# Kernel optimization log

Hardware: AMD Instinct MI355X
Metric: run time of the kernel (lower is better)

## Reference

```python
import jax, jax.numpy as jnp
import numpy as np

EPS = 1e-5
B, F, C, H, L, S = 8192, 128, 256, 512, 4, 10


def _gelu(x):
    return jax.nn.gelu(x, approximate=False)  # torch nn.GELU default = exact erf


def _ln(x, g, b):
    m = jnp.mean(x, axis=-1, keepdims=True)
    v = jnp.var(x, axis=-1, keepdims=True)  # biased, matches torch LayerNorm
    return (x - m) / jnp.sqrt(v + EPS) * g + b


def setup_inputs() -> dict:
    key = jax.random.key(0)
    ks = iter(jax.random.split(key, 40))

    def w(shape, fan_in):
        return jax.random.normal(next(ks), shape, jnp.float32) / np.float32(np.sqrt(fan_in))

    def z0(*s):
        return jnp.zeros(s, jnp.float32)

    return dict(
        x=jax.random.normal(next(ks), (B, F), jnp.float32),
        context=jax.random.normal(next(ks), (B, C), jnp.float32),
        u=jax.random.normal(next(ks), (S, B, F), jnp.float32),
        Wi=w((F, H), F), bi=z0(H),
        Wt1=w((1, H), 1), bt1=z0(H), Wt2=w((H, H), H), bt2=z0(H),
        Wc1=w((C, 2 * H), C), bc1=z0(2 * H), Wc2=w((2 * H, H), 2 * H), bc2=z0(H),
        Wv=w((L, H, H), H), bv=z0(L, H), Woa=w((L, H, H), H), boa=z0(L, H),
        g1=jnp.ones((L, H), jnp.float32), be1=z0(L, H),
        Wm1=w((L, H, 4 * H), H), bm1=z0(L, 4 * H),
        Wm2=w((L, 4 * H, H), 4 * H), bm2=z0(L, H),
        g2=jnp.ones((L, H), jnp.float32), be2=z0(L, H),
        Wcv=w((L, H, H), H), bcv=z0(L, H), Wco=w((L, H, H), H), bco=z0(L, H),
        scale=0.5 * jnp.ones((L,), jnp.float32),
        Wp1=w((H, H), H), bp1=z0(H), Wp2=w((H, F), H), bp2=z0(F),
    )


def _forward(x, context, u, Wi, bi, Wt1, bt1, Wt2, bt2, Wc1, bc1, Wc2, bc2,
             Wv, bv, Woa, boa, g1, be1, Wm1, bm1, Wm2, bm2, g2, be2,
             Wcv, bcv, Wco, bco, scale, Wp1, bp1, Wp2, bp2):
    n_steps = u.shape[0]
    dt = 1.0 / n_steps
    nb = x.shape[0]
    nl = Wv.shape[0]

    # context projection, computed once as in torch
    ctx = _gelu(context @ Wc1 + bc1) @ Wc2 + bc2  # [B,H]
    # seq_len==1 cross-attention: softmax over a single key == 1, so the output
    # is out_proj(v_proj(ctx)) and does not depend on x -> precompute per layer.
    vctx = jnp.einsum('bh,lhk->lbk', ctx, Wcv) + bcv[:, None, :]    # [L,B,H]
    xatt = jnp.einsum('lbh,lhk->lbk', vctx, Wco) + bco[:, None, :]  # [L,B,H]

    def vel(z, t):
        tt = jnp.clip(t, 0.0, 1.0)[:, None]                          # [B,1]
        h = z @ Wi + bi + (_gelu(tt @ Wt1 + bt1) @ Wt2 + bt2)        # [B,H]
        for l in range(nl):
            # seq_len==1 self-attention collapses to out_proj(v_proj(h))
            attn = (h @ Wv[l] + bv[l]) @ Woa[l] + boa[l]
            h = _ln(h + attn, g1[l], be1[l])
            mlp = _gelu(h @ Wm1[l] + bm1[l]) @ Wm2[l] + bm2[l]
            h = _ln(h + mlp, g2[l], be2[l])
            h = h + scale[l] * xatt[l]
        return _gelu(h @ Wp1 + bp1) @ Wp2 + bp2                      # [B,F]

    def step(carry, inp):
        z, ld = carry
        t_val, u_k = inp
        t = jnp.full((nb,), t_val, jnp.float32)
        zs = jax.lax.stop_gradient(z)  # matches z.detach()/leaf z_req in torch
        v, Ju = jax.jvp(lambda zz: vel(zz, t), (zs,), (u_k,))
        ld = ld + jnp.sum(u_k * Ju, axis=-1) * dt  # Hutchinson u^T J u
        return (zs + v * dt, ld), None

    ts = jnp.arange(n_steps, dtype=jnp.float32) * dt
    (z, log_det), _ = jax.lax.scan(step, (x, jnp.zeros((nb,), jnp.float32)), (ts, u))
    return z, log_det


def reference(x, context, u, Wi, bi, Wt1, bt1, Wt2, bt2, Wc1, bc1, Wc2, bc2,
              Wv, bv, Woa, boa, g1, be1, Wm1, bm1, Wm2, bm2, g2, be2,
              Wcv, bcv, Wco, bco, scale, Wp1, bp1, Wp2, bp2):
    return _forward(x, context, u, Wi, bi, Wt1, bt1, Wt2, bt2, Wc1, bc1, Wc2, bc2,
                    Wv, bv, Woa, boa, g1, be1, Wm1, bm1, Wm2, bm2, g2, be2,
                    Wcv, bcv, Wco, bco, scale, Wp1, bp1, Wp2, bp2)
```

## Files before the change

### kernel.cpp

```cpp
#include <hip/hip_runtime.h>
#include <math.h>

using floatx16 = __attribute__((ext_vector_type(16))) float;
using bf16x8   = __attribute__((ext_vector_type(8))) __bf16;
using ushort8  = __attribute__((ext_vector_type(8))) unsigned short;

__device__ __forceinline__ float b2f(unsigned short u) {
  unsigned v = ((unsigned)u) << 16; float f; __builtin_memcpy(&f, &v, 4); return f;
}
__device__ __forceinline__ unsigned short f2b(float f) {
  unsigned u; __builtin_memcpy(&u, &f, 4);
  u += 0x7fffu + ((u >> 16) & 1u);
  return (unsigned short)(u >> 16);
}
__device__ __forceinline__ float gelu_f(float x) {
  return 0.5f * x * (1.0f + erff(x * 0.7071067811865475f));
}
__device__ __forceinline__ float wred(float v) {
  #pragma unroll
  for (int off = 32; off > 0; off >>= 1) v += __shfl_xor(v, off, 64);
  return v;
}
__device__ __forceinline__ floatx16 zero16() {
  floatx16 z;
  #pragma unroll
  for (int e = 0; e < 16; e++) z[e] = 0.f;
  return z;
}

#define SWZS(r, c) (((r) << 5) + ((((c) ^ ((r) & 3))) << 3))

template<int MODE>
__global__ __launch_bounds__(256) void gemm_bt_k(
    const unsigned short* __restrict__ A, const unsigned short* __restrict__ Bt,
    void* __restrict__ C, const float* __restrict__ bias,
    const float* __restrict__ bias2, int M, int N, int K)
{
  __shared__ unsigned short As[2 * 128 * 32];
  __shared__ unsigned short Bs[2 * 128 * 32];
  const int tid  = threadIdx.x;
  const int lane = tid & 63;
  const int wave = tid >> 6;

  int bx = blockIdx.x, by = blockIdx.y;
  if ((gridDim.y & 7) == 0) {
    int lin = by * gridDim.x + bx;
    int xcd = lin & 7;
    int w   = lin >> 3;
    by = xcd * (gridDim.y >> 3) + w / gridDim.x;
    bx = w % gridDim.x;
  }
  const int row0 = by * 128;
  const int col0 = bx * 128;

  const int r0 = lane >> 2;
  const int cj = lane & 3;
  const unsigned short* Ag = A  + (size_t)(row0 + wave * 32 + r0) * K + cj * 8;
  const unsigned short* Bg = Bt + (size_t)(col0 + wave * 32 + r0) * K + cj * 8;
  const int aw0 = SWZS(wave * 32 + r0, cj);

  const int wr = wave >> 1, wc = wave & 1;
  const int m32 = lane & 31;
  const int hi  = lane >> 5;

  floatx16 acc[2][2];
  acc[0][0] = zero16(); acc[0][1] = zero16();
  acc[1][0] = zero16(); acc[1][1] = zero16();

  ushort8 ra0, ra1, rb0, rb1;
  ra0 = *(const ushort8*)(Ag);
  ra1 = *(const ushort8*)(Ag + (size_t)16 * K);
  rb0 = *(const ushort8*)(Bg);
  rb1 = *(const ushort8*)(Bg + (size_t)16 * K);

  int p = 0;
  for (int k0 = 0; k0 < K; k0 += 32) {
    unsigned short* Ab = &As[p * 4096];
    unsigned short* Bb = &Bs[p * 4096];
    *(ushort8*)(Ab + aw0)            = ra0;
    *(ushort8*)(Ab + aw0 + 16 * 32)  = ra1;
    *(ushort8*)(Bb + aw0)            = rb0;
    *(ushort8*)(Bb + aw0 + 16 * 32)  = rb1;
    __syncthreads();
    if (k0 + 32 < K) {
      ra0 = *(const ushort8*)(Ag + k0 + 32);
      ra1 = *(const ushort8*)(Ag + (size_t)16 * K + k0 + 32);
      rb0 = *(const ushort8*)(Bg + k0 + 32);
      rb1 = *(const ushort8*)(Bg + (size_t)16 * K + k0 + 32);
    }
    bf16x8 af[2][2], bfr[2][2];
    #pragma unroll
    for (int i = 0; i < 2; i++)
      #pragma unroll
      for (int h = 0; h < 2; h++)
        af[i][h] = *(const bf16x8*)&Ab[SWZS(wr * 64 + i * 32 + m32, 2 * h + hi)];
    #pragma unroll
    for (int j = 0; j < 2; j++)
      #pragma unroll
      for (int h = 0; h < 2; h++)
        bfr[j][h] = *(const bf16x8*)&Bb[SWZS(wc * 64 + j * 32 + m32, 2 * h + hi)];
    #pragma unroll
    for (int h = 0; h < 2; h++)
      #pragma unroll
      for (int i = 0; i < 2; i++)
        #pragma unroll
        for (int j = 0; j < 2; j++)
          acc[i][j] = __builtin_amdgcn_mfma_f32_32x32x16_bf16(af[i][h], bfr[j][h], acc[i][j], 0, 0, 0);
    p ^= 1;
  }

  #pragma unroll
  for (int j = 0; j < 2; j++) {
    int col = col0 + wc * 64 + j * 32 + m32;
    float bb = bias ? bias[col] : 0.f;
    if (MODE >= 2) { if (bias2) bb += bias2[col]; }
    #pragma unroll
    for (int i = 0; i < 2; i++) {
      int rb = row0 + wr * 64 + i * 32 + 4 * hi;
      if (MODE == 3) {
        #pragma unroll
        for (int pr = 0; pr < 8; pr++) {
          int re = rb + 2 * (pr & 1) + 8 * (pr >> 1);
          float pv = acc[i][j][2 * pr] + bb;
          float tv = acc[i][j][2 * pr + 1];
          float cdf = 0.5f * (1.0f + erff(pv * 0.7071067811865475f));
          float pdf = 0.3989422804014327f * expf(-0.5f * pv * pv);
          ((unsigned short*)C)[(size_t)re * N + col]       = f2b(pv * cdf);
          ((unsigned short*)C)[(size_t)(re + 1) * N + col] = f2b((cdf + pv * pdf) * tv);
        }
      } else {
        #pragma unroll
        for (int reg = 0; reg < 16; reg++) {
          int row = rb + (reg & 3) + 8 * (reg >> 2);
          float v = acc[i][j][reg];
          if (MODE == 0 || MODE == 1) v += bb;
          if (MODE == 2) { if ((reg & 1) == 0) v += bb; }
          if (MODE == 1) v = gelu_f(v);
          ((unsigned short*)C)[(size_t)row * N + col] = f2b(v);
        }
      }
    }
  }
}

__global__ __launch_bounds__(256, 2) void gemm_wide3_k(
    const unsigned short* __restrict__ A, const unsigned short* __restrict__ Bt,
    unsigned short* __restrict__ C, const float* __restrict__ bias,
    int M, int N, int K)
{
  __shared__ unsigned short As[2 * 128 * 32];
  __shared__ unsigned short Bs[2 * 256 * 32];
  const int tid  = threadIdx.x;
  const int lane = tid & 63;
  const int wave = tid >> 6;

  int bx = blockIdx.x, by = blockIdx.y;
  if ((gridDim.y & 7) == 0) {
    int lin = by * gridDim.x + bx;
    int xcd = lin & 7;
    int w   = lin >> 3;
    by = xcd * (gridDim.y >> 3) + w / gridDim.x;
    bx = w % gridDim.x;
  }
  const int row0 = by * 128;
  const int col0 = bx * 256;

  const int r0 = lane >> 2;
  const int cj = lane & 3;
  const unsigned short* Ag = A  + (size_t)(row0 + wave * 32 + r0) * K + cj * 8;
  const unsigned short* Bg = Bt + (size_t)(col0 + wave * 64 + r0) * K + cj * 8;
  const int awr = wave * 32 + r0;
  const int bwr = wave * 64 + r0;

  const int wr = wave >> 1, wc = wave & 1;
  const int m32 = lane & 31;
  const int hi  = lane >> 5;

  floatx16 acc[2][4];
  #pragma unroll
  for (int i = 0; i < 2; i++)
    #pragma unroll
    for (int j = 0; j < 4; j++) acc[i][j] = zero16();

  ushort8 ra0, ra1, rbv[4];
  ra0 = *(const ushort8*)(Ag);
  ra1 = *(const ushort8*)(Ag + (size_t)16 * K);
  #pragma unroll
  for (int t = 0; t < 4; t++)
    rbv[t] = *(const ushort8*)(Bg + (size_t)16 * t * K);

  int p = 0;
  for (int k0 = 0; k0 < K; k0 += 32) {
    unsigned short* Ab = &As[p * 4096];
    unsigned short* Bb = &Bs[p * 8192];
    *(ushort8*)&Ab[SWZS(awr, cj)]      = ra0;
    *(ushort8*)&Ab[SWZS(awr + 16, cj)] = ra1;
    #pragma unroll
    for (int t = 0; t < 4; t++)
      *(ushort8*)&Bb[SWZS(bwr + 16 * t, cj)] = rbv[t];
    __syncthreads();
    if (k0 + 32 < K) {
      ra0 = *(const ushort8*)(Ag + k0 + 32);
      ra1 = *(const ushort8*)(Ag + (size_t)16 * K + k0 + 32);
      #pragma unroll
      for (int t = 0; t < 4; t++)
        rbv[t] = *(const ushort8*)(Bg + (size_t)16 * t * K + k0 + 32);
    }
    bf16x8 af[2][2], bfr[4][2];
    #pragma unroll
    for (int i = 0; i < 2; i++)
      #pragma unroll
      for (int h = 0; h < 2; h++)
        af[i][h] = *(const bf16x8*)&Ab[SWZS(wr * 64 + i * 32 + m32, 2 * h + hi)];
    #pragma unroll
    for (int j = 0; j < 4; j++)
      #pragma unroll
      for (int h = 0; h < 2; h++)
        bfr[j][h] = *(const bf16x8*)&Bb[SWZS(wc * 128 + j * 32 + m32, 2 * h + hi)];
    #pragma unroll
    for (int h = 0; h < 2; h++)
      #pragma unroll
      for (int i = 0; i < 2; i++)
        #pragma unroll
        for (int j = 0; j < 4; j++)
          acc[i][j] = __builtin_amdgcn_mfma_f32_32x32x16_bf16(af[i][h], bfr[j][h], acc[i][j], 0, 0, 0);
    p ^= 1;
  }

  #pragma unroll
  for (int j = 0; j < 4; j++) {
    int col = col0 + wc * 128 + j * 32 + m32;
    float bb = bias[col];
    #pragma unroll
    for (int i = 0; i < 2; i++) {
      int rb = row0 + wr * 64 + i * 32 + 4 * hi;
      #pragma unroll
      for (int pr = 0; pr < 8; pr++) {
        int re = rb + 2 * (pr & 1) + 8 * (pr >> 1);
        float pv = acc[i][j][2 * pr] + bb;
        float tv = acc[i][j][2 * pr + 1];
        float cdf = 0.5f * (1.0f + erff(pv * 0.7071067811865475f));
        float pdf = 0.3989422804014327f * expf(-0.5f * pv * pv);
        C[(size_t)re * N + col]       = f2b(pv * cdf);
        C[(size_t)(re + 1) * N + col] = f2b((cdf + pv * pdf) * tv);
      }
    }
  }
}

__global__ __launch_bounds__(256) void gemm_vout_k(
    const unsigned short* __restrict__ A, const unsigned short* __restrict__ Bt,
    const float* __restrict__ bias, const float* __restrict__ u_cur,
    const float* __restrict__ u_next, float* __restrict__ zf,
    float* __restrict__ ldb, unsigned short* __restrict__ Abuf,
    int K, float dtv)
{
  constexpr int N = 128;
  __shared__ unsigned short As[2 * 128 * 32];
  __shared__ unsigned short Bs[2 * 128 * 32];
  __shared__ float red[64][2];
  const int tid = threadIdx.x, lane = tid & 63, wave = tid >> 6;
  const int row0 = blockIdx.x * 128;

  const int r0 = lane >> 2;
  const int cj = lane & 3;
  const unsigned short* Ag = A  + (size_t)(row0 + wave * 32 + r0) * K + cj * 8;
  const unsigned short* Bg = Bt + (size_t)(wave * 32 + r0) * K + cj * 8;
  const int aw0 = SWZS(wave * 32 + r0, cj);

  const int wr = wave >> 1, wc = wave & 1;
  const int m32 = lane & 31;
  const int hi  = lane >> 5;

  floatx16 acc[2][2];
  acc[0][0] = zero16(); acc[0][1] = zero16();
  acc[1][0] = zero16(); acc[1][1] = zero16();

  ushort8 ra0, ra1, rb0, rb1;
  ra0 = *(const ushort8*)(Ag);
  ra1 = *(const ushort8*)(Ag + (size_t)16 * K);
  rb0 = *(const ushort8*)(Bg);
  rb1 = *(const ushort8*)(Bg + (size_t)16 * K);

  int p = 0;
  for (int k0 = 0; k0 < K; k0 += 32) {
    unsigned short* Ab = &As[p * 4096];
    unsigned short* Bb = &Bs[p * 4096];
    *(ushort8*)(Ab + aw0)           = ra0;
    *(ushort8*)(Ab + aw0 + 16 * 32) = ra1;
    *(ushort8*)(Bb + aw0)           = rb0;
    *(ushort8*)(Bb + aw0 + 16 * 32) = rb1;
    __syncthreads();
    if (k0 + 32 < K) {
      ra0 = *(const ushort8*)(Ag + k0 + 32);
      ra1 = *(const ushort8*)(Ag + (size_t)16 * K + k0 + 32);
      rb0 = *(const ushort8*)(Bg + k0 + 32);
      rb1 = *(const ushort8*)(Bg + (size_t)16 * K + k0 + 32);
    }
    bf16x8 af[2][2], bfr[2][2];
    #pragma unroll
    for (int i = 0; i < 2; i++)
      #pragma unroll
      for (int h = 0; h < 2; h++)
        af[i][h] = *(const bf16x8*)&Ab[SWZS(wr * 64 + i * 32 + m32, 2 * h + hi)];
    #pragma unroll
    for (int j = 0; j < 2; j++)
      #pragma unroll
      for (int h = 0; h < 2; h++)
        bfr[j][h] = *(const bf16x8*)&Bb[SWZS(wc * 64 + j * 32 + m32, 2 * h + hi)];
    #pragma unroll
    for (int h = 0; h < 2; h++)
      #pragma unroll
      for (int i = 0; i < 2; i++)
        #pragma unroll
        for (int j = 0; j < 2; j++)
          acc[i][j] = __builtin_amdgcn_mfma_f32_32x32x16_bf16(af[i][h], bfr[j][h], acc[i][j], 0, 0, 0);
    p ^= 1;
  }

  #pragma unroll
  for (int i = 0; i < 2; i++) {
    #pragma unroll
    for (int pr = 0; pr < 8; pr++) {
      int re_loc = wr * 64 + i * 32 + 4 * hi + 2 * (pr & 1) + 8 * (pr >> 1);
      size_t growe = (size_t)(row0 + re_loc);
      size_t b = growe >> 1;
      float dacc = 0.f;
      #pragma unroll
      for (int j = 0; j < 2; j++) {
        int col = wc * 64 + j * 32 + m32;
        float v  = acc[i][j][2 * pr] + bias[col];
        float Ju = acc[i][j][2 * pr + 1];
        float z = zf[b * N + col] + v * dtv;
        zf[b * N + col] = z;
        Abuf[growe * N + col] = f2b(z);
        if (u_next) Abuf[(growe + 1) * N + col] = f2b(u_next[b * N + col]);
        dacc += u_cur[b * N + col] * Ju;
      }
      #pragma unroll
      for (int off = 1; off <= 16; off <<= 1) dacc += __shfl_xor(dacc, off, 64);
      if (m32 == 0) red[re_loc >> 1][wc] = dacc;
    }
  }
  __syncthreads();
  if (tid < 64) ldb[(row0 >> 1) + tid] += (red[tid][0] + red[tid][1]) * dtv;
}

__global__ __launch_bounds__(256) void ln_jvp_k(
    unsigned short* h, const unsigned short* __restrict__ r,
    const float* __restrict__ g, const float* __restrict__ be,
    const unsigned short* __restrict__ xatt, const float* __restrict__ sc_p,
    int Bhalf, int H)
{
  int gw = (int)((blockIdx.x * blockDim.x + threadIdx.x) >> 6);
  int lane = threadIdx.x & 63;
  if (gw >= Bhalf) return;
  int c0 = lane * 8;
  size_t op = (size_t)(2 * gw) * H + c0;
  size_t ot = op + H;
  ushort8 hp = *(const ushort8*)&h[op];
  ushort8 ht = *(const ushort8*)&h[ot];
  ushort8 rp = *(const ushort8*)&r[op];
  ushort8 rt = *(const ushort8*)&r[ot];
  float xv[8], dv[8];
  float s1 = 0.f, s2 = 0.f, sd = 0.f;
  #pragma unroll
  for (int j = 0; j < 8; j++) {
    xv[j] = b2f(hp[j]) + b2f(rp[j]);
    dv[j] = b2f(ht[j]) + b2f(rt[j]);
    s1 += xv[j]; s2 += xv[j] * xv[j]; sd += dv[j];
  }
  s1 = wred(s1); s2 = wred(s2); sd = wred(sd);
  float inv = 1.0f / (float)H;
  float m = s1 * inv;
  float var = s2 * inv - m * m;
  float rstd = rsqrtf(var + 1e-5f);
  float dm = sd * inv;
  float c = 0.f;
  #pragma unroll
  for (int j = 0; j < 8; j++) c += (xv[j] - m) * dv[j];
  c = wred(c);
  float cm = c * inv * rstd;
  float sl = sc_p ? *sc_p : 0.f;
  ushort8 oy, od;
  #pragma unroll
  for (int j = 0; j < 8; j++) {
    float xh = (xv[j] - m) * rstd;
    float gg = g[c0 + j];
    float y = xh * gg + be[c0 + j];
    if (xatt) y += sl * b2f(xatt[(size_t)gw * H + c0 + j]);
    float dy = gg * rstd * (dv[j] - dm - xh * cm);
    oy[j] = f2b(y); od[j] = f2b(dy);
  }
  *(ushort8*)&h[op] = oy;
  *(ushort8*)&h[ot] = od;
}

__global__ void transpose_cast_k(const float* __restrict__ W,
                                 unsigned short* __restrict__ Wt, int K, int N)
{
  __shared__ float tile[32][33];
  size_t off = (size_t)blockIdx.z * K * N;
  const float* Wp = W + off;
  unsigned short* Wtp = Wt + off;
  int bx = blockIdx.x, by = blockIdx.y;
  int tx = threadIdx.x, ty = threadIdx.y;
  #pragma unroll
  for (int i = ty; i < 32; i += 8)
    tile[i][tx] = Wp[(size_t)(by * 32 + i) * N + bx * 32 + tx];
  __syncthreads();
  #pragma unroll
  for (int i = ty; i < 32; i += 8)
    Wtp[(size_t)(bx * 32 + i) * K + by * 32 + tx] = f2b(tile[tx][i]);
}

__global__ __launch_bounds__(256) void zero_k(float* __restrict__ p, int n) {
  int i = (int)(blockIdx.x * blockDim.x + threadIdx.x);
  if (i < n) p[i] = 0.f;
}

__global__ __launch_bounds__(256) void combine_bias_k(
    const float* __restrict__ bvp, const float* __restrict__ Wb,
    const float* __restrict__ bo, float* __restrict__ bout, int H)
{
  int out = blockIdx.x * blockDim.x + threadIdx.x;
  int l   = blockIdx.y;
  int kc  = blockIdx.z;
  const float* A2 = Wb + (size_t)l * H * H;
  float s = (kc == 0) ? bo[(size_t)l * H + out] : 0.f;
  int kend = (kc + 1) * 64;
  for (int k = kc * 64; k < kend; k++) s += bvp[(size_t)l * H + k] * A2[(size_t)k * H + out];
  atomicAdd(&bout[(size_t)l * H + out], s);
}

__global__ __launch_bounds__(256) void cast_k(const float* __restrict__ in,
                                              unsigned short* __restrict__ out, size_t n) {
  size_t i = blockIdx.x * blockDim.x + threadIdx.x;
  if (i < n) out[i] = f2b(in[i]);
}

__global__ __launch_bounds__(512) void temb_all_k(
    const float* __restrict__ Wt1, const float* __restrict__ bt1,
    const float* __restrict__ Wt2, const float* __restrict__ bt2,
    float dtv, float* __restrict__ tvecs, int H)
{
  __shared__ float e[512];
  int j = threadIdx.x;
  float t = fminf(fmaxf((float)blockIdx.x * dtv, 0.f), 1.f);
  e[j] = gelu_f(t * Wt1[j] + bt1[j]);
  __syncthreads();
  float s = bt2[j];
  for (int k = 0; k < H; k++) s += e[k] * Wt2[(size_t)k * H + j];
  tvecs[(size_t)blockIdx.x * H + j] = s;
}

__global__ __launch_bounds__(256) void init_k(
    const float* __restrict__ x, const float* __restrict__ u0,
    float* __restrict__ zf, float* __restrict__ ld,
    unsigned short* __restrict__ Abuf, int BF, int Bsz, int F)
{
  int i = (int)(blockIdx.x * blockDim.x + threadIdx.x);
  if (i < BF) {
    int r = i / F, c = i - r * F;
    float v = x[i];
    zf[i] = v;
    Abuf[(size_t)(2 * r) * F + c]     = f2b(v);
    Abuf[(size_t)(2 * r + 1) * F + c] = f2b(u0[i]);
  }
  if (i < Bsz) ld[i] = 0.f;
}

__global__ __launch_bounds__(256) void final_k(
    const float* __restrict__ zf, const float* __restrict__ ld,
    float* __restrict__ out, int BF, int Bsz)
{
  int i = (int)(blockIdx.x * blockDim.x + threadIdx.x);
  if (i < BF) out[i] = zf[i];
  if (i < Bsz) out[BF + i] = ld[i];
}

extern "C" void kernel_launch(void* const* d_in, const int* in_sizes, int n_in,
                              void* d_out, int out_size, void* d_ws, size_t ws_size,
                              hipStream_t stream) {
  constexpr int B = 8192, F = 128, C = 256, H = 512, L = 4, S = 10;
  constexpr int B2 = 2 * B;
  constexpr int BF = B * F;
  const float dtv = 1.0f / S;

  const float* x    = (const float*)d_in[0];
  const float* ctxI = (const float*)d_in[1];
  const float* u    = (const float*)d_in[2];
  const float* Wi   = (const float*)d_in[3];
  const float* bi   = (const float*)d_in[4];
  const float* Wt1  = (const float*)d_in[5];
  const float* bt1  = (const float*)d_in[6];
  const float* Wt2  = (const float*)d_in[7];
  const float* bt2  = (const float*)d_in[8];
  const float* Wc1  = (const float*)d_in[9];
  const float* bc1  = (const float*)d_in[10];
  const float* Wc2  = (const float*)d_in[11];
  const float* bc2  = (const float*)d_in[12];
  const float* Wv   = (const float*)d_in[13];
  const float* bv   = (const float*)d_in[14];
  const float* Woa  = (const float*)d_in[15];
  const float* boa  = (const float*)d_in[16];
  const float* g1   = (const float*)d_in[17];
  const float* be1  = (const float*)d_in[18];
  const float* Wm1  = (const float*)d_in[19];
  const float* bm1  = (const float*)d_in[20];
  const float* Wm2  = (const float*)d_in[21];
  const float* bm2  = (const float*)d_in[22];
  const float* g2   = (const float*)d_in[23];
  const float* be2  = (const float*)d_in[24];
  const float* Wcv  = (const float*)d_in[25];
  const float* bcv  = (const float*)d_in[26];
  const float* Wco  = (const float*)d_in[27];
  const float* bco  = (const float*)d_in[28];
  const float* scal = (const float*)d_in[29];
  const float* Wp1  = (const float*)d_in[30];
  const float* bp1  = (const float*)d_in[31];
  const float* Wp2  = (const float*)d_in[32];
  const float* bp2  = (const float*)d_in[33];

  char* wp = (char*)d_ws;
  auto alloc = [&](size_t bytes) -> void* {
    void* r = (void*)wp;
    wp += (bytes + 255) & ~(size_t)255;
    return r;
  };
  unsigned short* wWit  = (unsigned short*)alloc((size_t)H * F * 2);
  unsigned short* wWc1t = (unsigned short*)alloc((size_t)2 * H * C * 2);
  unsigned short* wWc2t = (unsigned short*)alloc((size_t)H * 2 * H * 2);
  unsigned short* wWvoT = (unsigned short*)alloc((size_t)L * H * H * 2);
  unsigned short* wCtxT = (unsigned short*)alloc((size_t)L * H * H * 2);
  unsigned short* wWm1t = (unsigned short*)alloc((size_t)L * 4 * H * H * 2);
  unsigned short* wWm2t = (unsigned short*)alloc((size_t)L * H * 4 * H * 2);
  unsigned short* wWp1t = (unsigned short*)alloc((size_t)H * H * 2);
  unsigned short* wWp2t = (unsigned short*)alloc((size_t)F * H * 2);
  unsigned short* wOaT  = (unsigned short*)alloc((size_t)L * H * H * 2);
  unsigned short* wCoT  = (unsigned short*)alloc((size_t)L * H * H * 2);
  unsigned short* wVb   = (unsigned short*)alloc((size_t)L * H * H * 2);
  unsigned short* wCvb  = (unsigned short*)alloc((size_t)L * H * H * 2);
  float* bcomb          = (float*)alloc((size_t)2 * L * H * 4);
  float* bvo  = bcomb;
  float* cbvo = bcomb + (size_t)L * H;
  float* tvecs          = (float*)alloc((size_t)S * H * 4);
  unsigned short* ctxc  = (unsigned short*)alloc((size_t)B * C * 2);
  unsigned short* Abuf  = (unsigned short*)alloc((size_t)B2 * F * 2);
  unsigned short* hbuf  = (unsigned short*)alloc((size_t)B2 * H * 2);
  unsigned short* tmp2  = (unsigned short*)alloc((size_t)B2 * H * 2);
  unsigned short* mbuf  = (unsigned short*)alloc((size_t)B2 * 4 * H * 2);
  unsigned short* xattb = (unsigned short*)alloc((size_t)L * B * H * 2);
  float* zf             = (float*)alloc((size_t)B * F * 4);
  float* ldb            = (float*)alloc((size_t)B * 4);
  (void)ws_size; (void)in_sizes; (void)n_in; (void)out_size;

  auto T = [&](const float* W, unsigned short* Wt, int K, int N, int Lz) {
    dim3 g(N / 32, K / 32, Lz);
    transpose_cast_k<<<g, dim3(32, 8), 0, stream>>>(W, Wt, K, N);
  };
  auto G = [&](int mode, const unsigned short* A, const unsigned short* Bt, void* Cc,
               const float* bias, const float* bias2, int M, int N, int K) {
    dim3 g(N / 128, M / 128);
    switch (mode) {
      case 0: gemm_bt_k<0><<<g, 256, 0, stream>>>(A, Bt, Cc, bias, bias2, M, N, K); break;
      case 1: gemm_bt_k<1><<<g, 256, 0, stream>>>(A, Bt, Cc, bias, bias2, M, N, K); break;
      case 2: gemm_bt_k<2><<<g, 256, 0, stream>>>(A, Bt, Cc, bias, bias2, M, N, K); break;
      case 3: gemm_bt_k<3><<<g, 256, 0, stream>>>(A, Bt, Cc, bias, bias2, M, N, K); break;
    }
  };

  T(Wi,  wWit,  F, H, 1);
  T(Wc1, wWc1t, C, 2 * H, 1);
  T(Wc2, wWc2t, 2 * H, H, 1);
  T(Wm1, wWm1t, H, 4 * H, L);
  T(Wm2, wWm2t, 4 * H, H, L);
  T(Wp1, wWp1t, H, H, 1);
  T(Wp2, wWp2t, H, F, 1);
  T(Woa, wOaT, H, H, L);
  T(Wco, wCoT, H, H, L);
  cast_k<<<((size_t)L * H * H + 255) / 256, 256, 0, stream>>>(Wv,  wVb,  (size_t)L * H * H);
  cast_k<<<((size_t)L * H * H + 255) / 256, 256, 0, stream>>>(Wcv, wCvb, (size_t)L * H * H);
  for (int l = 0; l < L; l++) {
    size_t o2 = (size_t)l * H * H;
    G(0, wOaT + o2, wVb  + o2, wWvoT + o2, nullptr, nullptr, H, H, H);
    G(0, wCoT + o2, wCvb + o2, wCtxT + o2, nullptr, nullptr, H, H, H);
  }
  zero_k<<<(2 * L * H + 255) / 256, 256, 0, stream>>>(bcomb, 2 * L * H);
  combine_bias_k<<<dim3(H / 256, L, H / 64), 256, 0, stream>>>(bv,  Woa, boa, bvo,  H);
  combine_bias_k<<<dim3(H / 256, L, H / 64), 256, 0, stream>>>(bcv, Wco, bco, cbvo, H);

  cast_k<<<(B * C + 255) / 256, 256, 0, stream>>>(ctxI, ctxc, (size_t)B * C);
  G(1, ctxc, wWc1t, mbuf, bc1, nullptr, B, 2 * H, C);
  G(0, mbuf, wWc2t, tmp2, bc2, nullptr, B, H, 2 * H);
  for (int l = 0; l < L; l++)
    G(0, tmp2, wCtxT + (size_t)l * H * H, xattb + (size_t)l * B * H,
      cbvo + l * H, nullptr, B, H, H);

  temb_all_k<<<S, H, 0, stream>>>(Wt1, bt1, Wt2, bt2, dtv, tvecs, H);
  init_k<<<(BF + 255) / 256, 256, 0, stream>>>(x, u, zf, ldb, Abuf, BF, B, F);

  for (int s = 0; s < S; s++) {
    G(2, Abuf, wWit, hbuf, bi, tvecs + (size_t)s * H, B2, H, F);
    for (int l = 0; l < L; l++) {
      size_t o2 = (size_t)l * H * H;
      size_t om = (size_t)l * 4 * H * H;
      G(2, hbuf, wWvoT + o2, tmp2, bvo + l * H, nullptr, B2, H, H);
      ln_jvp_k<<<B / 4, 256, 0, stream>>>(hbuf, tmp2, g1 + l * H, be1 + l * H,
                                          nullptr, nullptr, B, H);
      gemm_wide3_k<<<dim3(4 * H / 256, B2 / 128), 256, 0, stream>>>(
          hbuf, wWm1t + om, mbuf, bm1 + (size_t)l * 4 * H, B2, 4 * H, H);
      G(2, mbuf, wWm2t + om, tmp2, bm2 + l * H, nullptr, B2, H, 4 * H);
      ln_jvp_k<<<B / 4, 256, 0, stream>>>(hbuf, tmp2, g2 + l * H, be2 + l * H,
                                          xattb + (size_t)l * B * H, scal + l, B, H);
    }
    G(3, hbuf, wWp1t, tmp2, bp1, nullptr, B2, H, H);
    const float* u_cur = u + (size_t)s * BF;
    const float* u_next = (s + 1 < S) ? u + (size_t)(s + 1) * BF : nullptr;
    gemm_vout_k<<<B2 / 128, 256, 0, stream>>>(
        tmp2, wWp2t, bp2, u_cur, u_next, zf, ldb, Abuf, H, dtv);
  }

  final_k<<<(BF + 255) / 256, 256, 0, stream>>>(zf, ldb, (float*)d_out, BF, B);
}
```

Baseline: 8.459 ms.

## Pre-tile weights into swizzled LDS image and load B via global_load_lds

```diff
diff --git a/kernel.cpp b/kernel.cpp
--- a/kernel.cpp
+++ b/kernel.cpp
@@ -27,10 +27,16 @@
   for (int e = 0; e < 16; e++) z[e] = 0.f;
   return z;
 }
+__device__ __forceinline__ void gload16(const unsigned short* g, unsigned short* l) {
+  __builtin_amdgcn_global_load_lds(
+      (__attribute__((address_space(1))) void*)(g),
+      (__attribute__((address_space(3))) void*)(l), 16, 0, 0);
+}
 
 #define SWZS(r, c) (((r) << 5) + ((((c) ^ ((r) & 3))) << 3))
 
-template<int MODE>
+
+template<int MODE, int IMG>
 __global__ __launch_bounds__(256) void gemm_bt_k(
     const unsigned short* __restrict__ A, const unsigned short* __restrict__ Bt,
     void* __restrict__ C, const float* __restrict__ bias,
@@ -55,9 +61,14 @@
 
   const int r0 = lane >> 2;
   const int cj = lane & 3;
-  const unsigned short* Ag = A  + (size_t)(row0 + wave * 32 + r0) * K + cj * 8;
-  const unsigned short* Bg = Bt + (size_t)(col0 + wave * 32 + r0) * K + cj * 8;
+  const unsigned short* Ag = A + (size_t)(row0 + wave * 32 + r0) * K + cj * 8;
   const int aw0 = SWZS(wave * 32 + r0, cj);
+
+  const int ks = K >> 5;
+  size_t bimg0 = 0;
+  const unsigned short* Bg = nullptr;
+  if (IMG) bimg0 = ((size_t)(col0 >> 7) * ks) * 4096 + (size_t)(wave * 2) * 512 + lane * 8;
+  else     Bg = Bt + (size_t)(col0 + wave * 32 + r0) * K + cj * 8;
 
   const int wr = wave >> 1, wc = wave & 1;
   const int m32 = lane & 31;
@@ -70,23 +81,38 @@
   ushort8 ra0, ra1, rb0, rb1;
   ra0 = *(const ushort8*)(Ag);
   ra1 = *(const ushort8*)(Ag + (size_t)16 * K);
-  rb0 = *(const ushort8*)(Bg);
-  rb1 = *(const ushort8*)(Bg + (size_t)16 * K);
+  if (IMG) {
+    gload16(Bt + bimg0,       &Bs[0] + (wave * 2) * 512);
+    gload16(Bt + bimg0 + 512, &Bs[0] + (wave * 2 + 1) * 512);
+  } else {
+    rb0 = *(const ushort8*)(Bg);
+    rb1 = *(const ushort8*)(Bg + (size_t)16 * K);
+  }
 
   int p = 0;
   for (int k0 = 0; k0 < K; k0 += 32) {
     unsigned short* Ab = &As[p * 4096];
     unsigned short* Bb = &Bs[p * 4096];
-    *(ushort8*)(Ab + aw0)            = ra0;
-    *(ushort8*)(Ab + aw0 + 16 * 32)  = ra1;
-    *(ushort8*)(Bb + aw0)            = rb0;
-    *(ushort8*)(Bb + aw0 + 16 * 32)  = rb1;
+    *(ushort8*)(Ab + aw0)           = ra0;
+    *(ushort8*)(Ab + aw0 + 16 * 32) = ra1;
+    if (!IMG) {
+      *(ushort8*)(Bb + aw0)           = rb0;
+      *(ushort8*)(Bb + aw0 + 16 * 32) = rb1;
+    }
     __syncthreads();
     if (k0 + 32 < K) {
+      if (IMG) {
+        size_t o = bimg0 + (size_t)((k0 >> 5) + 1) * 4096;
+        unsigned short* Bn = &Bs[(p ^ 1) * 4096];
+        gload16(Bt + o,       Bn + (wave * 2) * 512);
+        gload16(Bt + o + 512, Bn + (wave * 2 + 1) * 512);
+      }
       ra0 = *(const ushort8*)(Ag + k0 + 32);
       ra1 = *(const ushort8*)(Ag + (size_t)16 * K + k0 + 32);
-      rb0 = *(const ushort8*)(Bg + k0 + 32);
-      rb1 = *(const ushort8*)(Bg + (size_t)16 * K + k0 + 32);
+      if (!IMG) {
+        rb0 = *(const ushort8*)(Bg + k0 + 32);
+        rb1 = *(const ushort8*)(Bg + (size_t)16 * K + k0 + 32);
+      }
     }
     bf16x8 af[2][2], bfr[2][2];
     #pragma unroll
@@ -112,8 +138,9 @@
   #pragma unroll
   for (int j = 0; j < 2; j++) {
     int col = col0 + wc * 64 + j * 32 + m32;
-    float bb = bias ? bias[col] : 0.f;
-    if (MODE >= 2) { if (bias2) bb += bias2[col]; }
+    float bb = 0.f;
+    if (MODE != 5) { if (bias) bb = bias[col]; }
+    if (MODE >= 2 && MODE != 5) { if (bias2) bb += bias2[col]; }
     #pragma unroll
     for (int i = 0; i < 2; i++) {
       int rb = row0 + wr * 64 + i * 32 + 4 * hi;
@@ -128,6 +155,16 @@
           ((unsigned short*)C)[(size_t)re * N + col]       = f2b(pv * cdf);
           ((unsigned short*)C)[(size_t)(re + 1) * N + col] = f2b((cdf + pv * pdf) * tv);
         }
+      } else if (MODE == 5) {
+        int kc = N >> 5;
+        #pragma unroll
+        for (int reg = 0; reg < 16; reg++) {
+          int row = rb + (reg & 3) + 8 * (reg >> 2);
+          size_t off = ((size_t)(row >> 7) * kc + (col >> 5)) * 4096
+                     + (size_t)((row & 127) << 5)
+                     + ((((col >> 3) & 3) ^ (row & 3)) << 3) + (col & 7);
+          ((unsigned short*)C)[off] = f2b(acc[i][j][reg]);
+        }
       } else {
         #pragma unroll
         for (int reg = 0; reg < 16; reg++) {
@@ -167,10 +204,12 @@
 
   const int r0 = lane >> 2;
   const int cj = lane & 3;
-  const unsigned short* Ag = A  + (size_t)(row0 + wave * 32 + r0) * K + cj * 8;
-  const unsigned short* Bg = Bt + (size_t)(col0 + wave * 64 + r0) * K + cj * 8;
-  const int awr = wave * 32 + r0;
-  const int bwr = wave * 64 + r0;
+  const unsigned short* Ag = A + (size_t)(row0 + wave * 32 + r0) * K + cj * 8;
+  const int awr = SWZS(wave * 32 + r0, cj);
+
+  const int ks = K >> 5;
+  const size_t bq0 = ((size_t)((col0 >> 7) + 0) * ks) * 4096 + (size_t)(wave * 2) * 512 + lane * 8;
+  const size_t bq1 = ((size_t)((col0 >> 7) + 1) * ks) * 4096 + (size_t)(wave * 2) * 512 + lane * 8;
 
   const int wr = wave >> 1, wc = wave & 1;
   const int m32 = lane & 31;
@@ -182,29 +221,32 @@
     #pragma unroll
     for (int j = 0; j < 4; j++) acc[i][j] = zero16();
 
-  ushort8 ra0, ra1, rbv[4];
+  ushort8 ra0, ra1;
   ra0 = *(const ushort8*)(Ag);
   ra1 = *(const ushort8*)(Ag + (size_t)16 * K);
-  #pragma unroll
-  for (int t = 0; t < 4; t++)
-    rbv[t] = *(const ushort8*)(Bg + (size_t)16 * t * K);
+  {
+    gload16(Bt + bq0,       &Bs[0] + (wave * 2) * 512);
+    gload16(Bt + bq0 + 512, &Bs[0] + (wave * 2 + 1) * 512);
+    gload16(Bt + bq1,       &Bs[0] + 4096 + (wave * 2) * 512);
+    gload16(Bt + bq1 + 512, &Bs[0] + 4096 + (wave * 2 + 1) * 512);
+  }
 
   int p = 0;
   for (int k0 = 0; k0 < K; k0 += 32) {
     unsigned short* Ab = &As[p * 4096];
     unsigned short* Bb = &Bs[p * 8192];
-    *(ushort8*)&Ab[SWZS(awr, cj)]      = ra0;
-    *(ushort8*)&Ab[SWZS(awr + 16, cj)] = ra1;
-    #pragma unroll
-    for (int t = 0; t < 4; t++)
-      *(ushort8*)&Bb[SWZS(bwr + 16 * t, cj)] = rbv[t];
+    *(ushort8*)&Ab[awr]           = ra0;
+    *(ushort8*)&Ab[awr + 16 * 32] = ra1;
     __syncthreads();
     if (k0 + 32 < K) {
+      size_t so = (size_t)((k0 >> 5) + 1) * 4096;
+      unsigned short* Bn = &Bs[(p ^ 1) * 8192];
+      gload16(Bt + bq0 + so,       Bn + (wave * 2) * 512);
+      gload16(Bt + bq0 + so + 512, Bn + (wave * 2 + 1) * 512);
+      gload16(Bt + bq1 + so,       Bn + 4096 + (wave * 2) * 512);
+      gload16(Bt + bq1 + so + 512, Bn + 4096 + (wave * 2 + 1) * 512);
       ra0 = *(const ushort8*)(Ag + k0 + 32);
       ra1 = *(const ushort8*)(Ag + (size_t)16 * K + k0 + 32);
-      #pragma unroll
-      for (int t = 0; t < 4; t++)
-        rbv[t] = *(const ushort8*)(Bg + (size_t)16 * t * K + k0 + 32);
     }
     bf16x8 af[2][2], bfr[4][2];
     #pragma unroll
@@ -264,9 +306,9 @@
 
   const int r0 = lane >> 2;
   const int cj = lane & 3;
-  const unsigned short* Ag = A  + (size_t)(row0 + wave * 32 + r0) * K + cj * 8;
-  const unsigned short* Bg = Bt + (size_t)(wave * 32 + r0) * K + cj * 8;
+  const unsigned short* Ag = A + (size_t)(row0 + wave * 32 + r0) * K + cj * 8;
   const int aw0 = SWZS(wave * 32 + r0, cj);
+  const size_t bimg0 = (size_t)(wave * 2) * 512 + lane * 8;
 
   const int wr = wave >> 1, wc = wave & 1;
   const int m32 = lane & 31;
@@ -276,11 +318,11 @@
   acc[0][0] = zero16(); acc[0][1] = zero16();
   acc[1][0] = zero16(); acc[1][1] = zero16();
 
-  ushort8 ra0, ra1, rb0, rb1;
+  ushort8 ra0, ra1;
   ra0 = *(const ushort8*)(Ag);
   ra1 = *(const ushort8*)(Ag + (size_t)16 * K);
-  rb0 = *(const ushort8*)(Bg);
-  rb1 = *(const ushort8*)(Bg + (size_t)16 * K);
+  gload16(Bt + bimg0,       &Bs[0] + (wave * 2) * 512);
+  gload16(Bt + bimg0 + 512, &Bs[0] + (wave * 2 + 1) * 512);
 
   int p = 0;
   for (int k0 = 0; k0 < K; k0 += 32) {
@@ -288,14 +330,14 @@
     unsigned short* Bb = &Bs[p * 4096];
     *(ushort8*)(Ab + aw0)           = ra0;
     *(ushort8*)(Ab + aw0 + 16 * 32) = ra1;
-    *(ushort8*)(Bb + aw0)           = rb0;
-    *(ushort8*)(Bb + aw0 + 16 * 32) = rb1;
     __syncthreads();
     if (k0 + 32 < K) {
+      size_t o = bimg0 + (size_t)((k0 >> 5) + 1) * 4096;
+      unsigned short* Bn = &Bs[(p ^ 1) * 4096];
+      gload16(Bt + o,       Bn + (wave * 2) * 512);
+      gload16(Bt + o + 512, Bn + (wave * 2 + 1) * 512);
       ra0 = *(const ushort8*)(Ag + k0 + 32);
       ra1 = *(const ushort8*)(Ag + (size_t)16 * K + k0 + 32);
-      rb0 = *(const ushort8*)(Bg + k0 + 32);
-      rb1 = *(const ushort8*)(Bg + (size_t)16 * K + k0 + 32);
     }
     bf16x8 af[2][2], bfr[2][2];
     #pragma unroll
@@ -394,6 +436,30 @@
   }
   *(ushort8*)&h[op] = oy;
   *(ushort8*)&h[ot] = od;
+}
+
+__global__ void transpose_cast_img_k(const float* __restrict__ W,
+                                     unsigned short* __restrict__ Wt, int K, int N)
+{
+  __shared__ float tile[32][33];
+  size_t offI = (size_t)blockIdx.z * K * N;
+  const float* Wp = W + offI;
+  unsigned short* Wtp = Wt + offI;
+  int bx = blockIdx.x, by = blockIdx.y;
+  int tx = threadIdx.x, ty = threadIdx.y;
+  int ks = K >> 5;
+  #pragma unroll
+  for (int i = ty; i < 32; i += 8)
+    tile[i][tx] = Wp[(size_t)(by * 32 + i) * N + bx * 32 + tx];
+  __syncthreads();
+  #pragma unroll
+  for (int i = ty; i < 32; i += 8) {
+    int n = bx * 32 + i;
+    int r = n & 127;
+    size_t off = ((size_t)(n >> 7) * ks + by) * 4096
+               + (size_t)(r << 5) + ((((tx >> 3) ^ (r & 3))) << 3) + (tx & 7);
+    Wtp[off] = f2b(tile[tx][i]);
+  }
 }
 
 __global__ void transpose_cast_k(const float* __restrict__ W,
@@ -555,6 +621,10 @@
   float* ldb            = (float*)alloc((size_t)B * 4);
   (void)ws_size; (void)in_sizes; (void)n_in; (void)out_size;
 
+  auto Timg = [&](const float* W, unsigned short* Wt, int K, int N, int Lz) {
+    dim3 g(N / 32, K / 32, Lz);
+    transpose_cast_img_k<<<g, dim3(32, 8), 0, stream>>>(W, Wt, K, N);
+  };
   auto T = [&](const float* W, unsigned short* Wt, int K, int N, int Lz) {
     dim3 g(N / 32, K / 32, Lz);
     transpose_cast_k<<<g, dim3(32, 8), 0, stream>>>(W, Wt, K, N);
@@ -563,28 +633,29 @@
                const float* bias, const float* bias2, int M, int N, int K) {
     dim3 g(N / 128, M / 128);
     switch (mode) {
-      case 0: gemm_bt_k<0><<<g, 256, 0, stream>>>(A, Bt, Cc, bias, bias2, M, N, K); break;
-      case 1: gemm_bt_k<1><<<g, 256, 0, stream>>>(A, Bt, Cc, bias, bias2, M, N, K); break;
-      case 2: gemm_bt_k<2><<<g, 256, 0, stream>>>(A, Bt, Cc, bias, bias2, M, N, K); break;
-      case 3: gemm_bt_k<3><<<g, 256, 0, stream>>>(A, Bt, Cc, bias, bias2, M, N, K); break;
+      case 0: gemm_bt_k<0, 1><<<g, 256, 0, stream>>>(A, Bt, Cc, bias, bias2, M, N, K); break;
+      case 1: gemm_bt_k<1, 1><<<g, 256, 0, stream>>>(A, Bt, Cc, bias, bias2, M, N, K); break;
+      case 2: gemm_bt_k<2, 1><<<g, 256, 0, stream>>>(A, Bt, Cc, bias, bias2, M, N, K); break;
+      case 3: gemm_bt_k<3, 1><<<g, 256, 0, stream>>>(A, Bt, Cc, bias, bias2, M, N, K); break;
+      case 5: gemm_bt_k<5, 0><<<g, 256, 0, stream>>>(A, Bt, Cc, bias, bias2, M, N, K); break;
     }
   };
 
-  T(Wi,  wWit,  F, H, 1);
-  T(Wc1, wWc1t, C, 2 * H, 1);
-  T(Wc2, wWc2t, 2 * H, H, 1);
-  T(Wm1, wWm1t, H, 4 * H, L);
-  T(Wm2, wWm2t, 4 * H, H, L);
-  T(Wp1, wWp1t, H, H, 1);
-  T(Wp2, wWp2t, H, F, 1);
+  Timg(Wi,  wWit,  F, H, 1);
+  Timg(Wc1, wWc1t, C, 2 * H, 1);
+  Timg(Wc2, wWc2t, 2 * H, H, 1);
+  Timg(Wm1, wWm1t, H, 4 * H, L);
+  Timg(Wm2, wWm2t, 4 * H, H, L);
+  Timg(Wp1, wWp1t, H, H, 1);
+  Timg(Wp2, wWp2t, H, F, 1);
   T(Woa, wOaT, H, H, L);
   T(Wco, wCoT, H, H, L);
   cast_k<<<((size_t)L * H * H + 255) / 256, 256, 0, stream>>>(Wv,  wVb,  (size_t)L * H * H);
   cast_k<<<((size_t)L * H * H + 255) / 256, 256, 0, stream>>>(Wcv, wCvb, (size_t)L * H * H);
   for (int l = 0; l < L; l++) {
     size_t o2 = (size_t)l * H * H;
-    G(0, wOaT + o2, wVb  + o2, wWvoT + o2, nullptr, nullptr, H, H, H);
-    G(0, wCoT + o2, wCvb + o2, wCtxT + o2, nullptr, nullptr, H, H, H);
+    G(5, wOaT + o2, wVb  + o2, wWvoT + o2, nullptr, nullptr, H, H, H);
+    G(5, wCoT + o2, wCvb + o2, wCtxT + o2, nullptr, nullptr, H, H, H);
   }
   zero_k<<<(2 * L * H + 255) / 256, 256, 0, stream>>>(bcomb, 2 * L * H);
   combine_bias_k<<<dim3(H / 256, L, H / 64), 256, 0, stream>>>(bv,  Woa, boa, bvo,  H);
```

Result: slower. 8.918 ms (+5.4%).

## Fuse residual LayerNorm-JVP epilogue into full-row GEMM kernel

Applied to the files above, without the earlier changes.

```diff
diff --git a/kernel.cpp b/kernel.cpp
--- a/kernel.cpp
+++ b/kernel.cpp
@@ -15,11 +15,6 @@
 }
 __device__ __forceinline__ float gelu_f(float x) {
   return 0.5f * x * (1.0f + erff(x * 0.7071067811865475f));
-}
-__device__ __forceinline__ float wred(float v) {
-  #pragma unroll
-  for (int off = 32; off > 0; off >>= 1) v += __shfl_xor(v, off, 64);
-  return v;
 }
 __device__ __forceinline__ floatx16 zero16() {
   floatx16 z;
@@ -143,6 +138,141 @@
   }
 }
 
+template<bool XATT>
+__global__ __launch_bounds__(256) void gemm_ln_k(
+    const unsigned short* __restrict__ A, const unsigned short* __restrict__ Bt,
+    unsigned short* __restrict__ h, const float* __restrict__ bias,
+    const float* __restrict__ g, const float* __restrict__ be,
+    const unsigned short* __restrict__ xatt, const float* __restrict__ sc_p,
+    int K)
+{
+  constexpr int N = 512;
+  __shared__ unsigned short As[2 * 64 * 32];
+  __shared__ unsigned short Bs[2 * 512 * 32];
+  __shared__ float red[32][2][4];
+  const int tid = threadIdx.x, lane = tid & 63, wave = tid >> 6;
+  const int row0 = blockIdx.x * 64;
+
+  const int r0 = lane >> 2;
+  const int cj = lane & 3;
+  const unsigned short* Ag = A + (size_t)(row0 + wave * 16 + r0) * K + cj * 8;
+  const int awA = SWZS(wave * 16 + r0, cj);
+  const unsigned short* Bg = Bt + (size_t)(wave * 128 + r0) * K + cj * 8;
+  const int bwr = wave * 128 + r0;
+
+  const int wr = wave >> 1, wc = wave & 1;
+  const int m32 = lane & 31;
+  const int hi  = lane >> 5;
+
+  floatx16 acc[8];
+  #pragma unroll
+  for (int j = 0; j < 8; j++) acc[j] = zero16();
+
+  ushort8 ra0, rbv[8];
+  ra0 = *(const ushort8*)(Ag);
+  #pragma unroll
+  for (int t = 0; t < 8; t++)
+    rbv[t] = *(const ushort8*)(Bg + (size_t)16 * t * K);
+
+  int p = 0;
+  for (int k0 = 0; k0 < K; k0 += 32) {
+    unsigned short* Ab = &As[p * 2048];
+    unsigned short* Bb = &Bs[p * 16384];
+    *(ushort8*)&Ab[awA] = ra0;
+    #pragma unroll
+    for (int t = 0; t < 8; t++)
+      *(ushort8*)&Bb[SWZS(bwr + 16 * t, cj)] = rbv[t];
+    __syncthreads();
+    if (k0 + 32 < K) {
+      ra0 = *(const ushort8*)(Ag + k0 + 32);
+      #pragma unroll
+      for (int t = 0; t < 8; t++)
+        rbv[t] = *(const ushort8*)(Bg + (size_t)16 * t * K + k0 + 32);
+    }
+    bf16x8 af[2], bfr[8][2];
+    #pragma unroll
+    for (int hh = 0; hh < 2; hh++)
+      af[hh] = *(const bf16x8*)&Ab[SWZS(wr * 32 + m32, 2 * hh + hi)];
+    #pragma unroll
+    for (int j = 0; j < 8; j++)
+      #pragma unroll
+      for (int hh = 0; hh < 2; hh++)
+        bfr[j][hh] = *(const bf16x8*)&Bs[p * 16384 + SWZS(wc * 256 + j * 32 + m32, 2 * hh + hi)];
+    #pragma unroll
+    for (int hh = 0; hh < 2; hh++)
+      #pragma unroll
+      for (int j = 0; j < 8; j++)
+        acc[j] = __builtin_amdgcn_mfma_f32_32x32x16_bf16(af[hh], bfr[j][hh], acc[j], 0, 0, 0);
+    p ^= 1;
+  }
+
+  float bc[8], gc[8], bec[8];
+  #pragma unroll
+  for (int j = 0; j < 8; j++) {
+    int col = wc * 256 + j * 32 + m32;
+    bc[j] = bias[col]; gc[j] = g[col]; bec[j] = be[col];
+  }
+
+  #pragma unroll
+  for (int pr = 0; pr < 8; pr++) {
+    int re = wr * 32 + 4 * hi + 2 * (pr & 1) + 8 * (pr >> 1);
+    size_t ge = (size_t)(row0 + re) * N;
+    float sx = 0.f, sxx = 0.f, sdv = 0.f, sxdv = 0.f;
+    #pragma unroll
+    for (int j = 0; j < 8; j++) {
+      int col = wc * 256 + j * 32 + m32;
+      float xp = acc[j][2 * pr]     + bc[j] + b2f(h[ge + col]);
+      float dv = acc[j][2 * pr + 1]         + b2f(h[ge + N + col]);
+      acc[j][2 * pr] = xp; acc[j][2 * pr + 1] = dv;
+      sx += xp; sxx += xp * xp; sdv += dv; sxdv += xp * dv;
+    }
+    #pragma unroll
+    for (int off = 1; off <= 16; off <<= 1) {
+      sx   += __shfl_xor(sx, off, 64);
+      sxx  += __shfl_xor(sxx, off, 64);
+      sdv  += __shfl_xor(sdv, off, 64);
+      sxdv += __shfl_xor(sxdv, off, 64);
+    }
+    if (m32 == 0) {
+      int pid = re >> 1;
+      red[pid][wc][0] = sx; red[pid][wc][1] = sxx;
+      red[pid][wc][2] = sdv; red[pid][wc][3] = sxdv;
+    }
+  }
+  __syncthreads();
+
+  const float inv = 1.0f / 512.0f;
+  float sl = 0.f;
+  if (XATT) sl = *sc_p;
+  #pragma unroll
+  for (int pr = 0; pr < 8; pr++) {
+    int re = wr * 32 + 4 * hi + 2 * (pr & 1) + 8 * (pr >> 1);
+    int pid = re >> 1;
+    float sx   = red[pid][0][0] + red[pid][1][0];
+    float sxx  = red[pid][0][1] + red[pid][1][1];
+    float sdv  = red[pid][0][2] + red[pid][1][2];
+    float sxdv = red[pid][0][3] + red[pid][1][3];
+    float m = sx * inv;
+    float var = sxx * inv - m * m;
+    float rstd = rsqrtf(var + 1e-5f);
+    float dm = sdv * inv;
+    float cm = (sxdv - m * sdv) * inv * rstd;
+    size_t ge = (size_t)(row0 + re) * N;
+    size_t bx_ = (size_t)((row0 + re) >> 1) * N;
+    #pragma unroll
+    for (int j = 0; j < 8; j++) {
+      int col = wc * 256 + j * 32 + m32;
+      float xp = acc[j][2 * pr], dv = acc[j][2 * pr + 1];
+      float xh = (xp - m) * rstd;
+      float y = xh * gc[j] + bec[j];
+      if (XATT) y += sl * b2f(xatt[bx_ + col]);
+      float dy = gc[j] * rstd * (dv - dm - xh * cm);
+      h[ge + col]     = f2b(y);
+      h[ge + N + col] = f2b(dy);
+    }
+  }
+}
+
 __global__ __launch_bounds__(256, 2) void gemm_wide3_k(
     const unsigned short* __restrict__ A, const unsigned short* __restrict__ Bt,
     unsigned short* __restrict__ C, const float* __restrict__ bias,
@@ -344,56 +474,6 @@
   }
   __syncthreads();
   if (tid < 64) ldb[(row0 >> 1) + tid] += (red[tid][0] + red[tid][1]) * dtv;
-}
-
-__global__ __launch_bounds__(256) void ln_jvp_k(
-    unsigned short* h, const unsigned short* __restrict__ r,
-    const float* __restrict__ g, const float* __restrict__ be,
-    const unsigned short* __restrict__ xatt, const float* __restrict__ sc_p,
-    int Bhalf, int H)
-{
-  int gw = (int)((blockIdx.x * blockDim.x + threadIdx.x) >> 6);
-  int lane = threadIdx.x & 63;
-  if (gw >= Bhalf) return;
-  int c0 = lane * 8;
-  size_t op = (size_t)(2 * gw) * H + c0;
-  size_t ot = op + H;
-  ushort8 hp = *(const ushort8*)&h[op];
-  ushort8 ht = *(const ushort8*)&h[ot];
-  ushort8 rp = *(const ushort8*)&r[op];
-  ushort8 rt = *(const ushort8*)&r[ot];
-  float xv[8], dv[8];
-  float s1 = 0.f, s2 = 0.f, sd = 0.f;
-  #pragma unroll
-  for (int j = 0; j < 8; j++) {
-    xv[j] = b2f(hp[j]) + b2f(rp[j]);
-    dv[j] = b2f(ht[j]) + b2f(rt[j]);
-    s1 += xv[j]; s2 += xv[j] * xv[j]; sd += dv[j];
-  }
-  s1 = wred(s1); s2 = wred(s2); sd = wred(sd);
-  float inv = 1.0f / (float)H;
-  float m = s1 * inv;
-  float var = s2 * inv - m * m;
-  float rstd = rsqrtf(var + 1e-5f);
-  float dm = sd * inv;
-  float c = 0.f;
-  #pragma unroll
-  for (int j = 0; j < 8; j++) c += (xv[j] - m) * dv[j];
-  c = wred(c);
-  float cm = c * inv * rstd;
-  float sl = sc_p ? *sc_p : 0.f;
-  ushort8 oy, od;
-  #pragma unroll
-  for (int j = 0; j < 8; j++) {
-    float xh = (xv[j] - m) * rstd;
-    float gg = g[c0 + j];
-    float y = xh * gg + be[c0 + j];
-    if (xatt) y += sl * b2f(xatt[(size_t)gw * H + c0 + j]);
-    float dy = gg * rstd * (dv[j] - dm - xh * cm);
-    oy[j] = f2b(y); od[j] = f2b(dy);
-  }
-  *(ushort8*)&h[op] = oy;
-  *(ushort8*)&h[ot] = od;
 }
 
 __global__ void transpose_cast_k(const float* __restrict__ W,
@@ -605,14 +685,14 @@
     for (int l = 0; l < L; l++) {
       size_t o2 = (size_t)l * H * H;
       size_t om = (size_t)l * 4 * H * H;
-      G(2, hbuf, wWvoT + o2, tmp2, bvo + l * H, nullptr, B2, H, H);
-      ln_jvp_k<<<B / 4, 256, 0, stream>>>(hbuf, tmp2, g1 + l * H, be1 + l * H,
-                                          nullptr, nullptr, B, H);
+      gemm_ln_k<false><<<B2 / 64, 256, 0, stream>>>(
+          hbuf, wWvoT + o2, hbuf, bvo + l * H, g1 + l * H, be1 + l * H,
+          nullptr, nullptr, H);
       gemm_wide3_k<<<dim3(4 * H / 256, B2 / 128), 256, 0, stream>>>(
           hbuf, wWm1t + om, mbuf, bm1 + (size_t)l * 4 * H, B2, 4 * H, H);
-      G(2, mbuf, wWm2t + om, tmp2, bm2 + l * H, nullptr, B2, H, 4 * H);
-      ln_jvp_k<<<B / 4, 256, 0, stream>>>(hbuf, tmp2, g2 + l * H, be2 + l * H,
-                                          xattb + (size_t)l * B * H, scal + l, B, H);
+      gemm_ln_k<true><<<B2 / 64, 256, 0, stream>>>(
+          mbuf, wWm2t + om, hbuf, bm2 + l * H, g2 + l * H, be2 + l * H,
+          xattb + (size_t)l * B * H, scal + l, 4 * H);
     }
     G(3, hbuf, wWp1t, tmp2, bp1, nullptr, B2, H, H);
     const float* u_cur = u + (size_t)s * BF;
```

Result: faster. 7.797 ms (-7.8%).
